# Kernel optimization log

Hardware: AMD Instinct MI355X
Metric: run time of the kernel (lower is better)

Reference implementation:

```python
import jax, jax.numpy as jnp
import numpy as np

INTRA_W, TYPE_W, INTER_W = 1.0, 0.5, 0.5
MARGIN, TAU, EPS = 1.0, 0.1, 1e-8
N, D = 200000, 256          # nodes, feature dim
NT, EPT = 4, 2048           # n types, edges per type
E = NT * EPT                # 8192 hyperedges
SAMP_PER_TYPE = 100         # max_edges_per_type for intra loss
MAX_PAIRS = 500             # inter-loss pair sample


def setup_inputs() -> dict:
    key = jax.random.key(0)
    k1, k2, k3, k4, k5 = jax.random.split(key, 5)
    z_nodes = jax.random.normal(k1, (N, D), dtype=jnp.float32)
    # deterministic variable edge sizes in [8, 56]
    sizes = 8 + (np.arange(E) * 7919) % 49
    M = int(sizes.sum())  # 262128
    member_edge_id = jnp.asarray(np.repeat(np.arange(E), sizes), dtype=jnp.int32)
    member_node_idx = jax.random.randint(k2, (M,), 0, N, dtype=jnp.int32)
    edge_type = jnp.asarray(np.repeat(np.arange(NT), EPT), dtype=jnp.int32)
    # intra-loss edge sampling: 100 edges per type (mimics torch.randperm sampling)
    perm = jax.random.permutation(k3, EPT)
    intra_sample = jnp.concatenate(
        [perm[:SAMP_PER_TYPE] + t * EPT for t in range(NT)]).astype(jnp.int32)
    # inter-loss pair sampling (mimics torch.randint + self-collision fixup)
    pair_idx1 = jax.random.randint(k4, (MAX_PAIRS,), 0, E, dtype=jnp.int32)
    pair_idx2 = jax.random.randint(k5, (MAX_PAIRS,), 0, E, dtype=jnp.int32)
    pair_idx2 = jnp.where(pair_idx1 == pair_idx2, (pair_idx2 + 1) % E, pair_idx2)
    return dict(z_nodes=z_nodes, member_node_idx=member_node_idx,
                member_edge_id=member_edge_id, edge_type=edge_type,
                intra_sample=intra_sample, pair_idx1=pair_idx1, pair_idx2=pair_idx2)


def reference(z_nodes, member_node_idx, member_edge_id, edge_type,
              intra_sample, pair_idx1, pair_idx2):
    # --- ragged segment mean: hyperedge embeddings ---
    gathered = z_nodes[member_node_idx]                               # [M, D]
    counts = jax.ops.segment_sum(jnp.ones_like(member_edge_id, jnp.float32),
                                 member_edge_id, num_segments=E)      # [E]
    edge_sum = jax.ops.segment_sum(gathered, member_edge_id, num_segments=E)
    edge_emb = edge_sum / counts[:, None]                             # [E, D]

    # --- B1: intra-hyperedge loss over sampled edges ---
    sq_dist = jnp.sum((gathered - edge_emb[member_edge_id]) ** 2, axis=-1)  # [M]
    per_edge = jax.ops.segment_sum(sq_dist, member_edge_id, num_segments=E) / counts
    intra = jnp.mean(per_edge[intra_sample])

    # --- B2: type contrastive InfoNCE ---
    z = edge_emb / jnp.linalg.norm(edge_emb, axis=-1, keepdims=True)  # [E, D]
    sim = jnp.matmul(z, z.T) / TAU                                    # [E, E]
    self_mask = jnp.eye(E, dtype=bool)
    exp_sim = jnp.exp(sim) * (~self_mask)
    denom = exp_sim.sum(axis=1)
    type_mask = (edge_type[None, :] == edge_type[:, None]) & ~self_mask
    numer = jnp.sum(exp_sim * type_mask, axis=1)
    per_row = -jnp.log((numer + EPS) / (denom + EPS))
    has_pos = type_mask.sum(axis=1) > 0
    type_loss = jnp.sum(jnp.where(has_pos, per_row, 0.0)) / jnp.maximum(
        has_pos.sum().astype(per_row.dtype), 1.0)

    # --- B3: inter-hyperedge margin loss on sampled pairs ---
    dist = jnp.linalg.norm(edge_emb[pair_idx1] - edge_emb[pair_idx2], axis=-1)
    inter = jnp.mean(jax.nn.relu(MARGIN - dist) ** 2)

    total = INTRA_W * intra + TYPE_W * type_loss + INTER_W * inter
    return jnp.stack([intra, type_loss, inter, total])
```

## Files before the change

kernel.cpp:

```cpp
#include <hip/hip_runtime.h>


#define DDIM 256
#define NTYPES 4
#define TAU_INV 10.0f
#define EPSV 1e-8f

#define COLSEG 512
#define NCT (COLSEG / 16)

typedef short v8s __attribute__((ext_vector_type(8)));
typedef float v4f __attribute__((ext_vector_type(4)));
typedef unsigned short ushort_t;

__device__ __forceinline__ int lower_bound_i(const int* __restrict__ a, int n, int key) {
  int lo = 0, hi = n;
  while (lo < hi) { int mid = (lo + hi) >> 1; if (a[mid] < key) lo = mid + 1; else hi = mid; }
  return lo;
}

__device__ __forceinline__ ushort_t f2bf(float f) {
  union { float f; unsigned u; } v; v.f = f;
  unsigned r = v.u + 0x7FFFu + ((v.u >> 16) & 1u);
  return (ushort_t)(r >> 16);
}

__device__ __forceinline__ float bf2f(ushort_t u) {
  union { unsigned u; float f; } v; v.u = ((unsigned)u) << 16;
  return v.f;
}

__global__ __launch_bounds__(256)
void boundary_kernel(const int* __restrict__ mei, int M, int E,
                     int* __restrict__ off, float* __restrict__ typeSums,
                     float* __restrict__ scalars) {
  int i = blockIdx.x * 256 + threadIdx.x;
  if (i < M - 1) {
    int a = mei[i], b = mei[i + 1];
    for (int e = a + 1; e <= b; ++e) off[e] = i + 1;
  }
  if (i == 0) { off[0] = 0; off[E] = M; }
  if (i < E * NTYPES) typeSums[i] = 0.f;
  if (i < 8) scalars[i] = 0.f;
}

__global__ __launch_bounds__(256)
void edge_kernel(const float* __restrict__ z, const int* __restrict__ mni,
                 const int* __restrict__ off, int M, int E,
                 ushort_t* __restrict__ zn, float* __restrict__ emb,
                 float* __restrict__ per_edge, float* __restrict__ selfArr) {
  __shared__ int shIdx[64];
  __shared__ float shAcc[1024];
  __shared__ float shRed[12];
  int e = blockIdx.x;
  int tid = threadIdx.x;

  int s = off[e];
  int t = off[e + 1];
  int cnt = t - s;
  if (tid < cnt) shIdx[tid] = mni[s + tid];
  __syncthreads();

  int group = tid >> 6, lane = tid & 63;
  float4 acc = make_float4(0.f, 0.f, 0.f, 0.f);
  float sq = 0.f;
  int m = group;
  for (; m + 12 < cnt; m += 16) {
    int n0 = shIdx[m], n1 = shIdx[m + 4], n2 = shIdx[m + 8], n3 = shIdx[m + 12];
    float4 v0 = *(const float4*)(z + (size_t)n0 * DDIM + lane * 4);
    float4 v1 = *(const float4*)(z + (size_t)n1 * DDIM + lane * 4);
    float4 v2 = *(const float4*)(z + (size_t)n2 * DDIM + lane * 4);
    float4 v3 = *(const float4*)(z + (size_t)n3 * DDIM + lane * 4);
    acc.x += v0.x; acc.y += v0.y; acc.z += v0.z; acc.w += v0.w;
    sq += v0.x * v0.x + v0.y * v0.y + v0.z * v0.z + v0.w * v0.w;
    acc.x += v1.x; acc.y += v1.y; acc.z += v1.z; acc.w += v1.w;
    sq += v1.x * v1.x + v1.y * v1.y + v1.z * v1.z + v1.w * v1.w;
    acc.x += v2.x; acc.y += v2.y; acc.z += v2.z; acc.w += v2.w;
    sq += v2.x * v2.x + v2.y * v2.y + v2.z * v2.z + v2.w * v2.w;
    acc.x += v3.x; acc.y += v3.y; acc.z += v3.z; acc.w += v3.w;
    sq += v3.x * v3.x + v3.y * v3.y + v3.z * v3.z + v3.w * v3.w;
  }
  for (; m < cnt; m += 4) {
    int n0 = shIdx[m];
    float4 v0 = *(const float4*)(z + (size_t)n0 * DDIM + lane * 4);
    acc.x += v0.x; acc.y += v0.y; acc.z += v0.z; acc.w += v0.w;
    sq += v0.x * v0.x + v0.y * v0.y + v0.z * v0.z + v0.w * v0.w;
  }

  *(float4*)(&shAcc[tid * 4]) = acc;
  __syncthreads();
  int d = tid;
  float total = shAcc[d] + shAcc[256 + d] + shAcc[512 + d] + shAcc[768 + d];
  float inv = 1.0f / (float)cnt;
  float mu = total * inv;
  emb[(size_t)e * DDIM + d] = mu;

  float a1 = sq, a2 = mu * mu;
  #pragma unroll
  for (int off2 = 32; off2 > 0; off2 >>= 1) {
    a1 += __shfl_down(a1, off2);
    a2 += __shfl_down(a2, off2);
  }
  if (lane == 0) { shRed[group] = a1; shRed[4 + group] = a2; }
  __syncthreads();
  if (tid == 0) {
    float sqT = shRed[0] + shRed[1] + shRed[2] + shRed[3];
    float musqT = shRed[4] + shRed[5] + shRed[6] + shRed[7];
    per_edge[e] = sqT * inv - musqT;
    shRed[8] = musqT;
  }
  __syncthreads();
  float rn = rsqrtf(shRed[8]);
  ushort_t znv = f2bf(mu * rn);
  zn[(size_t)e * DDIM + d] = znv;

  float zq = bf2f(znv);
  float a3 = zq * zq;
  #pragma unroll
  for (int off2 = 32; off2 > 0; off2 >>= 1) a3 += __shfl_down(a3, off2);
  if (lane == 0) shRed[group] = a3;
  __syncthreads();
  if (tid == 0)
    selfArr[e] = __expf(TAU_INV * (shRed[0] + shRed[1] + shRed[2] + shRed[3]));
}

__global__ __launch_bounds__(256, 2)
void gemm_kernel(const ushort_t* __restrict__ zn, const int* __restrict__ edge_type,
                 int E, float* __restrict__ typeSums) {
  int tid = threadIdx.x;
  int lane = tid & 63, wave = tid >> 6;
  int quad = lane >> 4, l15 = lane & 15;
  int rb = blockIdx.y;
  int cs = blockIdx.x;
  int row0 = rb * 256 + wave * 64;
  int c0 = cs * COLSEG;
  int T = edge_type[c0];

  v8s aF[4][8];
  #pragma unroll
  for (int rt = 0; rt < 4; ++rt) {
    const ushort_t* base = zn + (size_t)(row0 + rt * 16 + l15) * DDIM + quad * 8;
    #pragma unroll
    for (int ks = 0; ks < 8; ++ks)
      aF[rt][ks] = *(const v8s*)(base + ks * 32);
  }

  float acc[4][4] = {};

  const ushort_t* bbase = zn + (size_t)(c0 + l15) * DDIM + quad * 8;

  v8s b0[8], b1[8];
  #pragma unroll
  for (int ks = 0; ks < 8; ++ks) b0[ks] = *(const v8s*)(bbase + ks * 32);

  auto step = [&](int ct, v8s (&cur)[8], v8s (&nxt)[8], bool pf) {
    if (pf) {
      const ushort_t* nb = bbase + (size_t)(ct + 1) * 16 * DDIM;
      #pragma unroll
      for (int ks = 0; ks < 8; ++ks) nxt[ks] = *(const v8s*)(nb + ks * 32);
    }
    v4f c[4];
    #pragma unroll
    for (int rt = 0; rt < 4; ++rt) c[rt] = (v4f){0.f, 0.f, 0.f, 0.f};
    #pragma unroll
    for (int ks = 0; ks < 8; ++ks)
      #pragma unroll
      for (int rt = 0; rt < 4; ++rt)
        c[rt] = __builtin_amdgcn_mfma_f32_16x16x32_bf16(aF[rt][ks], cur[ks], c[rt], 0, 0, 0);
    #pragma unroll
    for (int rt = 0; rt < 4; ++rt)
      #pragma unroll
      for (int rr = 0; rr < 4; ++rr)
        acc[rt][rr] += __expf(c[rt][rr] * TAU_INV);
  };

  for (int ct = 0; ct < NCT; ct += 2) {
    step(ct, b0, b1, true);
    step(ct + 1, b1, b0, ct + 2 < NCT);
  }

  #pragma unroll
  for (int rt = 0; rt < 4; ++rt) {
    #pragma unroll
    for (int rr = 0; rr < 4; ++rr) {
      float v = acc[rt][rr];
      v += __shfl_xor(v, 1);
      v += __shfl_xor(v, 2);
      v += __shfl_xor(v, 4);
      v += __shfl_xor(v, 8);
      if (l15 == 0) {
        int row = row0 + rt * 16 + quad * 4 + rr;
        atomicAdd(&typeSums[row * NTYPES + T], v);
      }
    }
  }
}

__global__ __launch_bounds__(256)
void tail_kernel(const float* __restrict__ emb, const float* __restrict__ per_edge,
                 const int* __restrict__ intra_sample, int nIntra,
                 const int* __restrict__ p1, const int* __restrict__ p2, int nPairs,
                 const float* __restrict__ typeSums, const float* __restrict__ selfArr,
                 const int* __restrict__ edge_type, int E, float* __restrict__ scalars) {
  __shared__ float sh[8];
  int b = blockIdx.x;
  int tid = threadIdx.x;
  int lane = tid & 63, wave = tid >> 6;
  int nRowBlocks = E / 256;

  if (b < nRowBlocks) {
    int row = b * 256 + tid;
    int t = edge_type[row];
    float self = selfArr[row];
    float s0 = typeSums[row * 4 + 0];
    float s1 = typeSums[row * 4 + 1];
    float s2 = typeSums[row * 4 + 2];
    float s3 = typeSums[row * 4 + 3];
    float denom = (s0 + s1 + s2 + s3) - self;
    float own = (t == 0) ? s0 : (t == 1) ? s1 : (t == 2) ? s2 : s3;
    float numer = own - self;
    float pr = 0.f, hp = 0.f;
    int cs = lower_bound_i(edge_type, E, t);
    int ce = lower_bound_i(edge_type, E, t + 1);
    if (ce - cs - 1 > 0) {
      hp = 1.f;
      pr = -__logf((numer + EPSV) / (denom + EPSV));
    }
    float a1 = pr, a2 = hp;
    #pragma unroll
    for (int off = 32; off > 0; off >>= 1) {
      a1 += __shfl_down(a1, off);
      a2 += __shfl_down(a2, off);
    }
    if (lane == 0) { sh[wave] = a1; sh[4 + wave] = a2; }
    __syncthreads();
    if (tid == 0) {
      atomicAdd(&scalars[2], sh[0] + sh[1] + sh[2] + sh[3]);
      atomicAdd(&scalars[3], sh[4] + sh[5] + sh[6] + sh[7]);
    }
  } else if (b == nRowBlocks) {
    float s = 0.f;
    for (int i = tid; i < nIntra; i += 256) s += per_edge[intra_sample[i]];
    #pragma unroll
    for (int off = 32; off > 0; off >>= 1) s += __shfl_down(s, off);
    if (lane == 0) sh[wave] = s;
    __syncthreads();
    if (tid == 0) atomicAdd(&scalars[0], sh[0] + sh[1] + sh[2] + sh[3]);
  } else {
    int p = (b - nRowBlocks - 1) * 4 + wave;
    if (p < nPairs) {
      int i1 = p1[p], i2 = p2[p];
      const float4* r1 = (const float4*)(emb + (size_t)i1 * DDIM);
      const float4* r2 = (const float4*)(emb + (size_t)i2 * DDIM);
      float4 x = r1[lane], y = r2[lane];
      float d0 = x.x - y.x, d1 = x.y - y.y, d2 = x.z - y.z, d3 = x.w - y.w;
      float s = d0 * d0 + d1 * d1 + d2 * d2 + d3 * d3;
      #pragma unroll
      for (int off = 32; off > 0; off >>= 1) s += __shfl_down(s, off);
      if (lane == 0) {
        float dist = sqrtf(s);
        float v = fmaxf(1.0f - dist, 0.0f);
        atomicAdd(&scalars[1], v * v);
      }
    }
  }
}

__global__ void finalize_kernel(const float* __restrict__ scalars, int nIntra, int nPairs,
                                float* __restrict__ out) {
  if (threadIdx.x == 0) {
    float intra = scalars[0] / (float)nIntra;
    float inter = scalars[1] / (float)nPairs;
    float typeL = scalars[2] / fmaxf(scalars[3], 1.f);
    out[0] = intra;
    out[1] = typeL;
    out[2] = inter;
    out[3] = 1.0f * intra + 0.5f * typeL + 0.5f * inter;
  }
}

extern "C" void kernel_launch(void* const* d_in, const int* in_sizes, int n_in,
                              void* d_out, int out_size, void* d_ws, size_t ws_size,
                              hipStream_t stream) {
  const float* z      = (const float*)d_in[0];
  const int* mni      = (const int*)d_in[1];
  const int* mei      = (const int*)d_in[2];
  const int* etype    = (const int*)d_in[3];
  const int* intra_s  = (const int*)d_in[4];
  const int* p1       = (const int*)d_in[5];
  const int* p2       = (const int*)d_in[6];
  int M      = in_sizes[1];
  int E      = in_sizes[3];
  int nIntra = in_sizes[4];
  int nPairs = in_sizes[5];

  char* ws = (char*)d_ws;
  ushort_t* zn    = (ushort_t*)ws;
  float* emb      = (float*)(ws + (size_t)E * DDIM * 2);
  float* per_edge = (float*)(ws + (size_t)E * DDIM * 6);
  float* typeSums = per_edge + E;
  float* selfArr  = typeSums + (size_t)E * NTYPES;
  float* scalars  = selfArr + E;
  int* off        = (int*)(scalars + 8);

  float* out = (float*)d_out;

  boundary_kernel<<<(M + 254) / 256, 256, 0, stream>>>(mei, M, E, off, typeSums, scalars);

  edge_kernel<<<E, 256, 0, stream>>>(z, mni, off, M, E, zn, emb, per_edge, selfArr);

  dim3 g(E / COLSEG, E / 256);
  gemm_kernel<<<g, 256, 0, stream>>>(zn, etype, E, typeSums);

  int nPB = (nPairs + 3) / 4;
  tail_kernel<<<E / 256 + 1 + nPB, 256, 0, stream>>>(
      emb, per_edge, intra_s, nIntra, p1, p2, nPairs,
      typeSums, selfArr, etype, E, scalars);

  finalize_kernel<<<1, 64, 0, stream>>>(scalars, nIntra, nPairs, out);
}
```

Before: 372.0 us.

## Stage B tiles in LDS via direct global-to-LDS loads in similarity GEMM

The similarity GEMM kernel now loads each 64-column B tile into shared memory with global_load_lds and shares it across the four waves, instead of each wave loading its own B fragments from global memory into registers. Every wave then reads its fragments from LDS, which cuts global/L2 traffic by up to 4x for the B operand. In exchange it adds two block barriers per tile, has no double buffering so loads and MFMA do not overlap, and the LDS fragment reads with a 512-byte row stride may bank-conflict. The launch-bounds occupancy hint of 2 blocks per SM is also removed.

```diff
diff --git a/kernel.cpp b/kernel.cpp
--- a/kernel.cpp
+++ b/kernel.cpp
@@ -7,7 +7,8 @@
 #define EPSV 1e-8f
 
 #define COLSEG 512
-#define NCT (COLSEG / 16)
+#define CTILE 64
+#define NT2 (COLSEG / CTILE)
 
 typedef short v8s __attribute__((ext_vector_type(8)));
 typedef float v4f __attribute__((ext_vector_type(4)));
@@ -28,6 +29,12 @@
 __device__ __forceinline__ float bf2f(ushort_t u) {
   union { unsigned u; float f; } v; v.u = ((unsigned)u) << 16;
   return v.f;
+}
+
+__device__ __forceinline__ void load_lds16(const ushort_t* g, ushort_t* l) {
+  __builtin_amdgcn_global_load_lds(
+      (const __attribute__((address_space(1))) unsigned int*)g,
+      (__attribute__((address_space(3))) unsigned int*)l, 16, 0, 0);
 }
 
 __global__ __launch_bounds__(256)
@@ -124,9 +131,11 @@
     selfArr[e] = __expf(TAU_INV * (shRed[0] + shRed[1] + shRed[2] + shRed[3]));
 }
 
-__global__ __launch_bounds__(256, 2)
+__global__ __launch_bounds__(256)
 void gemm_kernel(const ushort_t* __restrict__ zn, const int* __restrict__ edge_type,
                  int E, float* __restrict__ typeSums) {
+  __shared__ __align__(16) ushort_t sB[CTILE * DDIM];
+
   int tid = threadIdx.x;
   int lane = tid & 63, wave = tid >> 6;
   int quad = lane >> 4, l15 = lane & 15;
@@ -147,36 +156,43 @@
 
   float acc[4][4] = {};
 
-  const ushort_t* bbase = zn + (size_t)(c0 + l15) * DDIM + quad * 8;
-
-  v8s b0[8], b1[8];
-  #pragma unroll
-  for (int ks = 0; ks < 8; ++ks) b0[ks] = *(const v8s*)(bbase + ks * 32);
-
-  auto step = [&](int ct, v8s (&cur)[8], v8s (&nxt)[8], bool pf) {
-    if (pf) {
-      const ushort_t* nb = bbase + (size_t)(ct + 1) * 16 * DDIM;
-      #pragma unroll
-      for (int ks = 0; ks < 8; ++ks) nxt[ks] = *(const v8s*)(nb + ks * 32);
-    }
-    v4f c[4];
-    #pragma unroll
-    for (int rt = 0; rt < 4; ++rt) c[rt] = (v4f){0.f, 0.f, 0.f, 0.f};
-    #pragma unroll
-    for (int ks = 0; ks < 8; ++ks)
+  for (int t = 0; t < NT2; ++t) {
+    const ushort_t* src = zn + (size_t)(c0 + t * CTILE) * DDIM;
+    #pragma unroll
+    for (int it = 0; it < 8; ++it) {
+      int f = it * 256 + tid;
+      load_lds16(src + f * 8, &sB[f * 8]);
+    }
+    __syncthreads();
+
+    #pragma unroll
+    for (int h = 0; h < 2; ++h) {
+      v4f c[4][2];
       #pragma unroll
       for (int rt = 0; rt < 4; ++rt)
-        c[rt] = __builtin_amdgcn_mfma_f32_16x16x32_bf16(aF[rt][ks], cur[ks], c[rt], 0, 0, 0);
-    #pragma unroll
-    for (int rt = 0; rt < 4; ++rt)
+        #pragma unroll
+        for (int ct = 0; ct < 2; ++ct)
+          c[rt][ct] = (v4f){0.f, 0.f, 0.f, 0.f};
+
       #pragma unroll
-      for (int rr = 0; rr < 4; ++rr)
-        acc[rt][rr] += __expf(c[rt][rr] * TAU_INV);
-  };
-
-  for (int ct = 0; ct < NCT; ct += 2) {
-    step(ct, b0, b1, true);
-    step(ct + 1, b1, b0, ct + 2 < NCT);
+      for (int ks = 0; ks < 8; ++ks) {
+        #pragma unroll
+        for (int ct = 0; ct < 2; ++ct) {
+          v8s b = *(const v8s*)(&sB[((h * 2 + ct) * 16 + l15) * DDIM + ks * 32 + quad * 8]);
+          #pragma unroll
+          for (int rt = 0; rt < 4; ++rt)
+            c[rt][ct] = __builtin_amdgcn_mfma_f32_16x16x32_bf16(aF[rt][ks], b, c[rt][ct], 0, 0, 0);
+        }
+      }
+      #pragma unroll
+      for (int rt = 0; rt < 4; ++rt)
+        #pragma unroll
+        for (int ct = 0; ct < 2; ++ct)
+          #pragma unroll
+          for (int rr = 0; rr < 4; ++rr)
+            acc[rt][rr] += __expf(c[rt][ct][rr] * TAU_INV);
+    }
+    __syncthreads();
   }
 
   #pragma unroll
```

Measured after the change: 348.6 us. -6.3%, faster.
